# Kernel optimization log

Measured on AMD Instinct MI355X. Metric: run time of the kernel, lower is better.

Reference implementation:

```python
import jax, jax.numpy as jnp
import numpy as np

N_HEADS = 16
HEAD_DIM = 64
THRESHOLD = 0.5
TAU = 12.5
N_FHN_STEPS = 2


def fhn_imex_step(v, w, I, a, b, dt, tau):
    # IMEX step of FitzHugh-Nagumo dynamics:
    #   explicit update for v (nonlinear), implicit for w (linear in w)
    #   dv/dt = v - v^3/3 - w + I
    #   dw/dt = (v + a - b*w) / tau
    v_new = v + dt * (v - v ** 3 / 3.0 - w + I)
    w_new = (w + (dt / tau) * (v_new + a)) / (1.0 + (dt / tau) * b)
    return v_new, w_new


def setup_inputs() -> dict:
    key = jax.random.key(0)
    k1, k2, k3 = jax.random.split(key, 3)
    B, T, D = 2, 2048, 1024
    x = jax.random.normal(k1, (B, T, D), dtype=jnp.float32)
    Wqkv = jax.random.normal(k2, (3 * D, D), dtype=jnp.float32) * 0.02
    Wout = jax.random.normal(k3, (D, D), dtype=jnp.float32) * 0.02
    a = jnp.float32(0.7)
    b = jnp.float32(0.8)
    dt = jnp.float32(1.0)
    return {"x": x, "Wqkv": Wqkv, "Wout": Wout, "a": a, "b": b, "dt": dt}


def reference(x, Wqkv, Wout, a, b, dt):
    B, T, D = x.shape
    H, hd = N_HEADS, HEAD_DIM
    qkv = x @ Wqkv.T                              # (B, T, 3D)
    qkv = qkv.reshape(B, T, 3, H, hd)             # 'b t (three h d)'
    q = qkv[:, :, 0].transpose(0, 2, 1, 3)        # (B, H, T, hd)
    k = qkv[:, :, 1].transpose(0, 2, 1, 3)
    v = qkv[:, :, 2].transpose(0, 2, 1, 3)

    scores = jnp.einsum('bhtd,bhsd->bhts', q, k) / np.sqrt(hd).astype(np.float32)
    causal = jnp.triu(jnp.ones((T, T), dtype=bool), k=1)
    scores = jnp.where(causal[None, None], -jnp.inf, scores)
    attn_probs = jax.nn.softmax(scores, axis=-1)  # (B, H, T, T); dropout=0 -> identity

    attn_energy = attn_probs.sum(axis=-1)                              # (B, H, T)
    stim_scale = jnp.maximum(jnp.abs(attn_energy).max(axis=-1, keepdims=True), 1e-6)
    stimulus_normed = attn_energy / stim_scale
    threshold_gate = jax.nn.sigmoid((jnp.abs(attn_energy) - THRESHOLD) * 10.0)
    I = stimulus_normed * (0.1 + 0.9 * threshold_gate)                 # (B, H, T)
    I = jnp.broadcast_to(I[..., None], (B, H, T, hd))                  # expand to head_dim

    v_state = jnp.zeros_like(I)
    w_state = jnp.zeros_like(I)
    for _ in range(N_FHN_STEPS):
        v_state, w_state = fhn_imex_step(v_state, w_state, I, a, b, dt, TAU)

    fhn_gate = jax.nn.sigmoid(v_state.mean(axis=-1))[..., None]        # (B, H, T, 1)
    attn_probs = attn_probs * (0.5 + 0.5 * fhn_gate)
    attn_probs = attn_probs / (attn_probs.sum(axis=-1, keepdims=True) + 1e-8)

    out = jnp.einsum('bhts,bhsd->bhtd', attn_probs, v)                 # (B, H, T, hd)
    out = out.transpose(0, 2, 1, 3).reshape(B, T, D)
    out = out @ Wout.T
    return out
```

## Files before the change

kernel.cpp:

```cpp
#include <hip/hip_runtime.h>

typedef unsigned short u16;
typedef __attribute__((ext_vector_type(8))) short bf16x8;
typedef __attribute__((ext_vector_type(4))) float f32x4;
typedef __attribute__((ext_vector_type(4))) unsigned short u16x4;
typedef __attribute__((ext_vector_type(2))) unsigned int u32x2;

__device__ __forceinline__ u16 f2bf(float f) {
    unsigned int u = __builtin_bit_cast(unsigned int, f);
    u += 0x7fffu + ((u >> 16) & 1u);
    return (u16)(u >> 16);
}

__device__ __forceinline__ float bf2f(u16 b) {
    unsigned int u = ((unsigned int)b) << 16;
    return __builtin_bit_cast(float, u);
}

__device__ __forceinline__ unsigned int cvt_pk_bf16(float lo, float hi) {
    unsigned int r;
    asm("v_cvt_pk_bf16_f32 %0, %1, %2" : "=v"(r) : "v"(lo), "v"(hi));
    return r;
}

__device__ __forceinline__ void gload_lds16(const u16* g, const u16* l) {
    __builtin_amdgcn_global_load_lds((const __attribute__((address_space(1))) void*)g,
                                     (__attribute__((address_space(3))) void*)l,
                                     16, 0, 0);
}

__global__ __launch_bounds__(256) void cvt_f32_bf16(const float* __restrict__ in,
                                                    u16* __restrict__ out, int n4) {
    int i = blockIdx.x * blockDim.x + threadIdx.x;
    int stride = gridDim.x * blockDim.x;
    for (; i < n4; i += stride) {
        float4 v = reinterpret_cast<const float4*>(in)[i];
        u16x4 o = { f2bf(v.x), f2bf(v.y), f2bf(v.z), f2bf(v.w) };
        reinterpret_cast<u16x4*>(out)[i] = o;
    }
}

template <typename OutT>
__global__ __launch_bounds__(256) void gemm_bt(const u16* __restrict__ A, const u16* __restrict__ B,
                                               OutT* __restrict__ C, int M, int N, int K) {
    __shared__ u16 ldsA[128 * 64];
    __shared__ u16 ldsB[128 * 64];
    const int tid = threadIdx.x;
    const int lane = tid & 63;
    const int wid = tid >> 6;
    const int wm = wid >> 1, wn = wid & 1;
    const int lq = lane & 15, lg = lane >> 4;

    const int nbn = N >> 7;
    const int id = blockIdx.x;
    const int idp = (id & 7) * ((int)gridDim.x >> 3) + (id >> 3);
    const int bm = (idp / nbn) * 128;
    const int bn = (idp % nbn) * 128;

    const u16* aSrc[4];
    const u16* bSrc[4];
    int dstOff[4];
#pragma unroll
    for (int j = 0; j < 4; ++j) {
        int item = j * 256 + tid;
        int row = item >> 3;
        int c16 = item & 7;
        aSrc[j] = A + (size_t)(bm + row) * K + c16 * 8;
        bSrc[j] = B + (size_t)(bn + row) * K + c16 * 8;
        dstOff[j] = (j * 256 + (tid & ~63)) * 16;
    }

    f32x4 acc[4][4] = {};
    for (int k0 = 0; k0 < K; k0 += 64) {
        if (k0) __syncthreads();
#pragma unroll
        for (int j = 0; j < 4; ++j) {
            gload_lds16(aSrc[j], (const u16*)((const char*)ldsA + dstOff[j]));
            gload_lds16(bSrc[j], (const u16*)((const char*)ldsB + dstOff[j]));
            aSrc[j] += 64;
            bSrc[j] += 64;
        }
        __syncthreads();
#pragma unroll
        for (int kk = 0; kk < 2; ++kk) {
            bf16x8 af[4], bfr[4];
#pragma unroll
            for (int m = 0; m < 4; ++m) {
                int row = wm * 64 + m * 16 + lq;
                af[m] = *(const bf16x8*)((const char*)ldsA + row * 128 + kk * 64 + lg * 16);
            }
#pragma unroll
            for (int n = 0; n < 4; ++n) {
                int row = wn * 64 + n * 16 + lq;
                bfr[n] = *(const bf16x8*)((const char*)ldsB + row * 128 + kk * 64 + lg * 16);
            }
#pragma unroll
            for (int m = 0; m < 4; ++m)
#pragma unroll
                for (int n = 0; n < 4; ++n)
                    acc[m][n] = __builtin_amdgcn_mfma_f32_16x16x32_bf16(af[m], bfr[n], acc[m][n], 0, 0, 0);
        }
    }

#pragma unroll
    for (int m = 0; m < 4; ++m) {
#pragma unroll
        for (int n = 0; n < 4; ++n) {
#pragma unroll
            for (int r = 0; r < 4; ++r) {
                int row = bm + wm * 64 + m * 16 + lg * 4 + r;
                int col = bn + wn * 64 + n * 16 + lq;
                float v = acc[m][n][r];
                if constexpr (sizeof(OutT) == 2)
                    C[(size_t)row * N + col] = (OutT)f2bf(v);
                else
                    C[(size_t)row * N + col] = (OutT)v;
            }
        }
    }
}

__global__ __launch_bounds__(256) void transpose_v(const u16* __restrict__ qkv, u16* __restrict__ vt) {
    __shared__ u16 tile[64][72];
    const int tb = blockIdx.x * 64;
    const int bh = blockIdx.y;
    const int b = bh >> 4, h = bh & 15;
    const u16* src = qkv + ((size_t)(b * 2048 + tb)) * 3072 + 2048 + h * 64;
    const int tid = threadIdx.x;
#pragma unroll
    for (int p = 0; p < 2; ++p) {
        int item = p * 256 + tid;
        int t = item >> 3, c = item & 7;
        bf16x8 v = *(const bf16x8*)(src + (size_t)t * 3072 + c * 8);
        *(bf16x8*)(&tile[t][c * 8]) = v;
    }
    __syncthreads();
    u16* dst = vt + ((size_t)bh * 64) * 2048 + tb;
#pragma unroll
    for (int p = 0; p < 2; ++p) {
        int item = p * 256 + tid;
        int d = item >> 3, tc = item & 7;
        bf16x8 o;
#pragma unroll
        for (int j = 0; j < 8; ++j) o[j] = (short)tile[tc * 8 + j][d];
        *(bf16x8*)(dst + (size_t)d * 2048 + tc * 8) = o;
    }
}

__global__ __launch_bounds__(256, 4) void fhn_attn(const u16* __restrict__ qkv, const u16* __restrict__ vt,
                                                   u16* __restrict__ attno) {
    __shared__ u16 kvbuf[2][2][64 * 64];
    __shared__ u16 plds[4][16][64];
    const int id = blockIdx.x;
    const int bh = (id & 7) * 4 + ((id >> 3) & 3);
    const int tile = id >> 5;
    const int qt = (bh & 1) ? tile : (31 - tile);
    const int b = bh >> 4, h = bh & 15;
    const int tid = threadIdx.x;
    const int w = tid >> 6;
    const int lane = tid & 63;
    const int lq = lane & 15, lg = lane >> 4;
    const int qlo = qt * 64 + w * 16;
    const int tq = qlo + lq;

    bf16x8 qf[2];
    {
        const u16* qrow = qkv + ((size_t)(b * 2048 + tq)) * 3072 + h * 64;
        qf[0] = *(const bf16x8*)(qrow + lg * 8);
        qf[1] = *(const bf16x8*)(qrow + 32 + lg * 8);
#pragma unroll
        for (int kk = 0; kk < 2; ++kk)
#pragma unroll
            for (int j = 0; j < 8; ++j)
                qf[kk][j] = (short)f2bf(bf2f((u16)qf[kk][j]) * 0.1803368801f);
    }

    const int it0 = tid, it1 = 256 + tid;
    const int r0 = it0 >> 3, g0 = (it0 & 7) ^ (r0 & 7);
    const int r1 = it1 >> 3, g1 = (it1 & 7) ^ (r1 & 7);
    const u16* kS0 = qkv + ((size_t)(b * 2048 + r0)) * 3072 + 1024 + h * 64 + g0 * 8;
    const u16* kS1 = qkv + ((size_t)(b * 2048 + r1)) * 3072 + 1024 + h * 64 + g1 * 8;
    const u16* vS0 = vt + ((size_t)bh * 64 + r0) * 2048 + g0 * 8;
    const u16* vS1 = vt + ((size_t)bh * 64 + r1) * 2048 + g1 * 8;
    const int d0 = (it0 & ~63) * 8;
    const int d1 = (it1 & ~63) * 8;

#define STAGE(buf)                                            \
    do {                                                      \
        gload_lds16(kS0, &kvbuf[buf][0][d0]);                 \
        gload_lds16(kS1, &kvbuf[buf][0][d1]);                 \
        gload_lds16(vS0, &kvbuf[buf][1][d0]);                 \
        gload_lds16(vS1, &kvbuf[buf][1][d1]);                 \
        kS0 += 64 * 3072; kS1 += 64 * 3072;                   \
        vS0 += 64; vS1 += 64;                                 \
    } while (0)

    const int nkv = qt + 1;
    float m_run = -1e30f, l_run = 0.f;
    f32x4 oacc[4] = {};
    int cur = 0;

    char* const pbase = (char*)&plds[w][0][0] + lq * 128;
    const int pswz = (lq & 7) << 4;

    STAGE(0);

    for (int jb = 0; jb < nkv; ++jb) {
        asm volatile("s_waitcnt vmcnt(0)" ::: "memory");
        __builtin_amdgcn_s_barrier();
        __builtin_amdgcn_sched_barrier(0);
        if (jb + 1 < nkv) STAGE(cur ^ 1);

        const u16* kb = kvbuf[cur][0];
        const u16* vb = kvbuf[cur][1];

        float p[4][4];
        __builtin_amdgcn_s_setprio(1);
#pragma unroll
        for (int st = 0; st < 4; ++st) {
            int row = st * 16 + lq;
            f32x4 sacc = {};
            sacc = __builtin_amdgcn_mfma_f32_16x16x32_bf16(
                *(const bf16x8*)(kb + row * 64 + ((lg ^ (row & 7)) * 8)), qf[0], sacc, 0, 0, 0);
            sacc = __builtin_amdgcn_mfma_f32_16x16x32_bf16(
                *(const bf16x8*)(kb + row * 64 + (((4 + lg) ^ (row & 7)) * 8)), qf[1], sacc, 0, 0, 0);
#pragma unroll
            for (int r = 0; r < 4; ++r) p[st][r] = sacc[r];
        }
        __builtin_amdgcn_s_setprio(0);

        bf16x8 vf[2][4];
#pragma unroll
        for (int c = 0; c < 2; ++c)
#pragma unroll
            for (int nd = 0; nd < 4; ++nd) {
                int row = nd * 16 + lq;
                vf[c][nd] = *(const bf16x8*)(vb + row * 64 + (((c * 4 + lg) ^ (row & 7)) * 8));
            }

        if (jb == qt) {
#pragma unroll
            for (int st = 0; st < 4; ++st)
#pragma unroll
                for (int r = 0; r < 4; ++r) {
                    int s = jb * 64 + st * 16 + lg * 4 + r;
                    if (s > tq) p[st][r] = -1e30f;
                }
        }

        float mst[4];
#pragma unroll
        for (int st = 0; st < 4; ++st)
            mst[st] = fmaxf(fmaxf(p[st][0], p[st][1]), fmaxf(p[st][2], p[st][3]));
        float mloc = fmaxf(fmaxf(mst[0], mst[1]), fmaxf(mst[2], mst[3]));
        mloc = fmaxf(mloc, __shfl_xor(mloc, 16));
        mloc = fmaxf(mloc, __shfl_xor(mloc, 32));

        if (!__all(mloc - m_run <= 8.0f)) {
            float mnew = fmaxf(m_run, mloc);
            float scp = exp2f(m_run - mnew);
            m_run = mnew;
            l_run *= scp;
            float f0 = __shfl(scp, lg * 4 + 0);
            float f1 = __shfl(scp, lg * 4 + 1);
            float f2_ = __shfl(scp, lg * 4 + 2);
            float f3 = __shfl(scp, lg * 4 + 3);
#pragma unroll
            for (int nd = 0; nd < 4; ++nd) {
                oacc[nd][0] *= f0; oacc[nd][1] *= f1;
                oacc[nd][2] *= f2_; oacc[nd][3] *= f3;
            }
        }

        float lst[4];
#pragma unroll
        for (int st = 0; st < 4; ++st) {
#pragma unroll
            for (int r = 0; r < 4; ++r)
                p[st][r] = exp2f(p[st][r] - m_run);
            lst[st] = (p[st][0] + p[st][1]) + (p[st][2] + p[st][3]);
            u32x2 pk = { cvt_pk_bf16(p[st][0], p[st][1]), cvt_pk_bf16(p[st][2], p[st][3]) };
            *(u32x2*)(pbase + ((st * 32 + lg * 8) ^ pswz)) = pk;
        }
        float lloc = (lst[0] + lst[1]) + (lst[2] + lst[3]);
        lloc += __shfl_xor(lloc, 16);
        lloc += __shfl_xor(lloc, 32);
        l_run += lloc;

        __builtin_amdgcn_s_setprio(1);
#pragma unroll
        for (int c = 0; c < 2; ++c) {
            bf16x8 pa = *(const bf16x8*)(pbase + ((c * 64 + lg * 16) ^ pswz));
#pragma unroll
            for (int nd = 0; nd < 4; ++nd)
                oacc[nd] = __builtin_amdgcn_mfma_f32_16x16x32_bf16(pa, vf[c][nd], oacc[nd], 0, 0, 0);
        }
        __builtin_amdgcn_s_setprio(0);

        cur ^= 1;
    }
#undef STAGE

    float li0 = 1.f / __shfl(l_run, lg * 4 + 0);
    float li1 = 1.f / __shfl(l_run, lg * 4 + 1);
    float li2 = 1.f / __shfl(l_run, lg * 4 + 2);
    float li3 = 1.f / __shfl(l_run, lg * 4 + 3);
#pragma unroll
    for (int nd = 0; nd < 4; ++nd) {
#pragma unroll
        for (int r = 0; r < 4; ++r) {
            int trow = qlo + lg * 4 + r;
            float li = (r == 0) ? li0 : (r == 1) ? li1 : (r == 2) ? li2 : li3;
            attno[((size_t)(b * 2048 + trow)) * 1024 + h * 64 + nd * 16 + lq] =
                f2bf(oacc[nd][r] * li);
        }
    }
}

extern "C" void kernel_launch(void* const* d_in, const int* in_sizes, int n_in,
                              void* d_out, int out_size, void* d_ws, size_t ws_size,
                              hipStream_t stream) {
    const float* x    = (const float*)d_in[0];
    const float* Wqkv = (const float*)d_in[1];
    const float* Wout = (const float*)d_in[2];
    float* out = (float*)d_out;

    char* ws = (char*)d_ws;
    u16* xb    = (u16*)(ws + 0);
    u16* wqkvb = (u16*)(ws + 8388608);
    u16* woutb = (u16*)(ws + 14680064);
    u16* qkvb  = (u16*)(ws + 16777216);
    u16* vtb   = (u16*)(ws + 41943040);
    u16* attno = (u16*)(ws + 50331648);

    cvt_f32_bf16<<<2048, 256, 0, stream>>>(x, xb, 4194304 / 4);
    cvt_f32_bf16<<<2048, 256, 0, stream>>>(Wqkv, wqkvb, 3145728 / 4);
    cvt_f32_bf16<<<1024, 256, 0, stream>>>(Wout, woutb, 1048576 / 4);

    gemm_bt<u16><<<768, 256, 0, stream>>>(xb, wqkvb, qkvb, 4096, 3072, 1024);

    transpose_v<<<dim3(32, 32), 256, 0, stream>>>(qkvb, vtb);

    fhn_attn<<<1024, 256, 0, stream>>>(qkvb, vtb, attno);

    gemm_bt<float><<<256, 256, 0, stream>>>(attno, woutb, out, 4096, 1024, 1024);
}
```

Baseline: 129.5 us.

## Split long causal attention query tiles across two blocks with merge kernel

The upper 16 query tiles of causal attention now have their KV range split in half between two blocks. Each half writes unnormalized partial outputs plus running max and sum to scratch buffers that reuse the workspace of the already-consumed bf16 x and Wqkv. A new merge kernel combines the two halves with log-sum-exp rescaling. This balances per-block work to cut the tail of the causal triangle, at the cost of an extra launch, scratch traffic, and a bf16 rounding of the partial outputs.

```diff
diff --git a/kernel.cpp b/kernel.cpp
--- a/kernel.cpp
+++ b/kernel.cpp
@@ -148,13 +148,31 @@
 }
 
 __global__ __launch_bounds__(256, 4) void fhn_attn(const u16* __restrict__ qkv, const u16* __restrict__ vt,
-                                                   u16* __restrict__ attno) {
+                                                   u16* __restrict__ attno,
+                                                   u16* __restrict__ pO, float* __restrict__ pML) {
     __shared__ u16 kvbuf[2][2][64 * 64];
     __shared__ u16 plds[4][16][64];
     const int id = blockIdx.x;
-    const int bh = (id & 7) * 4 + ((id >> 3) & 3);
-    const int tile = id >> 5;
-    const int qt = (bh & 1) ? tile : (31 - tile);
+    const int xcd = id & 7;
+    const int u = id >> 3;
+    const int bh = xcd * 4 + (u & 3);
+    const int unit = u >> 2;
+    int qt, jb0, jb1, sidx;
+    bool split;
+    if (unit < 32) {
+        qt = 31 - (unit >> 1);
+        sidx = unit & 1;
+        split = true;
+        int n = qt + 1, hh = (n + 1) >> 1;
+        jb0 = sidx ? hh : 0;
+        jb1 = sidx ? n : hh;
+    } else {
+        qt = 47 - unit;
+        sidx = 0;
+        split = false;
+        jb0 = 0;
+        jb1 = qt + 1;
+    }
     const int b = bh >> 4, h = bh & 15;
     const int tid = threadIdx.x;
     const int w = tid >> 6;
@@ -178,10 +196,10 @@
     const int it0 = tid, it1 = 256 + tid;
     const int r0 = it0 >> 3, g0 = (it0 & 7) ^ (r0 & 7);
     const int r1 = it1 >> 3, g1 = (it1 & 7) ^ (r1 & 7);
-    const u16* kS0 = qkv + ((size_t)(b * 2048 + r0)) * 3072 + 1024 + h * 64 + g0 * 8;
-    const u16* kS1 = qkv + ((size_t)(b * 2048 + r1)) * 3072 + 1024 + h * 64 + g1 * 8;
-    const u16* vS0 = vt + ((size_t)bh * 64 + r0) * 2048 + g0 * 8;
-    const u16* vS1 = vt + ((size_t)bh * 64 + r1) * 2048 + g1 * 8;
+    const u16* kS0 = qkv + ((size_t)(b * 2048 + jb0 * 64 + r0)) * 3072 + 1024 + h * 64 + g0 * 8;
+    const u16* kS1 = qkv + ((size_t)(b * 2048 + jb0 * 64 + r1)) * 3072 + 1024 + h * 64 + g1 * 8;
+    const u16* vS0 = vt + ((size_t)bh * 64 + r0) * 2048 + jb0 * 64 + g0 * 8;
+    const u16* vS1 = vt + ((size_t)bh * 64 + r1) * 2048 + jb0 * 64 + g1 * 8;
     const int d0 = (it0 & ~63) * 8;
     const int d1 = (it1 & ~63) * 8;
 
@@ -195,7 +213,6 @@
         vS0 += 64; vS1 += 64;                                 \
     } while (0)
 
-    const int nkv = qt + 1;
     float m_run = -1e30f, l_run = 0.f;
     f32x4 oacc[4] = {};
     int cur = 0;
@@ -205,11 +222,11 @@
 
     STAGE(0);
 
-    for (int jb = 0; jb < nkv; ++jb) {
+    for (int jb = jb0; jb < jb1; ++jb) {
         asm volatile("s_waitcnt vmcnt(0)" ::: "memory");
         __builtin_amdgcn_s_barrier();
         __builtin_amdgcn_sched_barrier(0);
-        if (jb + 1 < nkv) STAGE(cur ^ 1);
+        if (jb + 1 < jb1) STAGE(cur ^ 1);
 
         const u16* kb = kvbuf[cur][0];
         const u16* vb = kvbuf[cur][1];
@@ -301,19 +318,68 @@
     }
 #undef STAGE
 
-    float li0 = 1.f / __shfl(l_run, lg * 4 + 0);
-    float li1 = 1.f / __shfl(l_run, lg * 4 + 1);
-    float li2 = 1.f / __shfl(l_run, lg * 4 + 2);
-    float li3 = 1.f / __shfl(l_run, lg * 4 + 3);
-#pragma unroll
-    for (int nd = 0; nd < 4; ++nd) {
-#pragma unroll
-        for (int r = 0; r < 4; ++r) {
-            int trow = qlo + lg * 4 + r;
-            float li = (r == 0) ? li0 : (r == 1) ? li1 : (r == 2) ? li2 : li3;
-            attno[((size_t)(b * 2048 + trow)) * 1024 + h * 64 + nd * 16 + lq] =
-                f2bf(oacc[nd][r] * li);
-        }
+    if (split) {
+        const int pidx = ((((bh << 4) | (qt - 16)) << 1) + sidx);
+        u16* obase = pO + (size_t)pidx * 4096;
+#pragma unroll
+        for (int nd = 0; nd < 4; ++nd)
+#pragma unroll
+            for (int r = 0; r < 4; ++r) {
+                int rt = w * 16 + lg * 4 + r;
+                obase[rt * 64 + nd * 16 + lq] = f2bf(oacc[nd][r]);
+            }
+        if (lg == 0) {
+            pML[pidx * 128 + w * 16 + lq] = m_run;
+            pML[pidx * 128 + 64 + w * 16 + lq] = l_run;
+        }
+    } else {
+        float li0 = 1.f / __shfl(l_run, lg * 4 + 0);
+        float li1 = 1.f / __shfl(l_run, lg * 4 + 1);
+        float li2 = 1.f / __shfl(l_run, lg * 4 + 2);
+        float li3 = 1.f / __shfl(l_run, lg * 4 + 3);
+#pragma unroll
+        for (int nd = 0; nd < 4; ++nd) {
+#pragma unroll
+            for (int r = 0; r < 4; ++r) {
+                int trow = qlo + lg * 4 + r;
+                float li = (r == 0) ? li0 : (r == 1) ? li1 : (r == 2) ? li2 : li3;
+                attno[((size_t)(b * 2048 + trow)) * 1024 + h * 64 + nd * 16 + lq] =
+                    f2bf(oacc[nd][r] * li);
+            }
+        }
+    }
+}
+
+__global__ __launch_bounds__(256) void attn_merge(const u16* __restrict__ pO, const float* __restrict__ pML,
+                                                  u16* __restrict__ attno) {
+    const int tilei = blockIdx.x;
+    const int bh = tilei >> 4, q16 = tilei & 15;
+    const int qt = 16 + q16;
+    const int b = bh >> 4, h = bh & 15;
+    const int p0 = tilei * 2, p1 = p0 + 1;
+    const int t = threadIdx.x;
+    const int rt = t >> 2;
+    const int c0 = (t & 3) * 16;
+
+    float m0 = pML[p0 * 128 + rt], l0 = pML[p0 * 128 + 64 + rt];
+    float m1 = pML[p1 * 128 + rt], l1 = pML[p1 * 128 + 64 + rt];
+    float M = fmaxf(m0, m1);
+    float a0 = exp2f(m0 - M), a1 = exp2f(m1 - M);
+    float inv = 1.f / (l0 * a0 + l1 * a1);
+    a0 *= inv; a1 *= inv;
+
+    const u16* O0 = pO + (size_t)p0 * 4096 + rt * 64 + c0;
+    const u16* O1 = pO + (size_t)p1 * 4096 + rt * 64 + c0;
+    u16* dst = attno + ((size_t)(b * 2048 + qt * 64 + rt)) * 1024 + h * 64 + c0;
+#pragma unroll
+    for (int half = 0; half < 2; ++half) {
+        bf16x8 v0 = *(const bf16x8*)(O0 + half * 8);
+        bf16x8 v1 = *(const bf16x8*)(O1 + half * 8);
+        bf16x8 o;
+#pragma unroll
+        for (int j = 0; j < 8; ++j)
+            o[j] = (short)f2bf(bf2f((u16)v0[j]) * a0 + bf2f((u16)v1[j]) * a1);
+        *(bf16x8*)(dst + half * 8) = o;
     }
 }
 
@@ -332,6 +398,8 @@
     u16* qkvb  = (u16*)(ws + 16777216);
     u16* vtb   = (u16*)(ws + 41943040);
     u16* attno = (u16*)(ws + 50331648);
+    u16* pO    = xb;
+    float* pML = (float*)wqkvb;
 
     cvt_f32_bf16<<<2048, 256, 0, stream>>>(x, xb, 4194304 / 4);
     cvt_f32_bf16<<<2048, 256, 0, stream>>>(Wqkv, wqkvb, 3145728 / 4);
@@ -341,7 +409,9 @@
 
     transpose_v<<<dim3(32, 32), 256, 0, stream>>>(qkvb, vtb);
 
-    fhn_attn<<<1024, 256, 0, stream>>>(qkvb, vtb, attno);
+    fhn_attn<<<1536, 256, 0, stream>>>(qkvb, vtb, attno, pO, pML);
+
+    attn_merge<<<512, 256, 0, stream>>>(pO, pML, attno);
 
     gemm_bt<float><<<256, 256, 0, stream>>>(attno, woutb, out, 4096, 1024, 1024);
 }
```

After: 129.9 us. Within noise of the previous version (+0.3%).
